# Optimization experiments

Hardware: AMD Instinct MI355X
Metric: run time of the kernel (lower is better)

## Reference

```python
import jax, jax.numpy as jnp
import numpy as np
import math

D_MODEL = 2048
B, S, PAST = 4, 2048, 2048


def setup_inputs() -> dict:
    key = jax.random.key(0)
    ks = jax.random.split(key, 8)
    scale = 0.02
    x = jax.random.normal(ks[0], (B, S, D_MODEL), dtype=jnp.float32)
    past_k = jax.random.normal(ks[1], (B, PAST, D_MODEL), dtype=jnp.float32)
    past_v = jax.random.normal(ks[2], (B, PAST, D_MODEL), dtype=jnp.float32)
    Wq = jax.random.normal(ks[3], (D_MODEL, D_MODEL), dtype=jnp.float32) * scale
    Wk = jax.random.normal(ks[4], (D_MODEL, D_MODEL), dtype=jnp.float32) * scale
    Wv = jax.random.normal(ks[5], (D_MODEL, D_MODEL), dtype=jnp.float32) * scale
    Wo = jax.random.normal(ks[6], (D_MODEL, D_MODEL), dtype=jnp.float32) * scale
    bq = jnp.zeros((D_MODEL,), jnp.float32)
    bk = jnp.zeros((D_MODEL,), jnp.float32)
    bv = jnp.zeros((D_MODEL,), jnp.float32)
    bo = jnp.zeros((D_MODEL,), jnp.float32)
    return {"x": x, "past_k": past_k, "past_v": past_v,
            "Wq": Wq, "bq": bq, "Wk": Wk, "bk": bk,
            "Wv": Wv, "bv": bv, "Wo": Wo, "bo": bo}


def reference(x, past_k, past_v, Wq, bq, Wk, bk, Wv, bv, Wo, bo):
    d_model = x.shape[-1]
    # torch Linear: y = x @ W.T + b; here W is stored [out, in] equivalently square
    q = jnp.einsum('bsd,ed->bse', x, Wq) + bq
    k = jnp.einsum('bsd,ed->bse', x, Wk) + bk
    v = jnp.einsum('bsd,ed->bse', x, Wv) + bv
    k_cache = jnp.concatenate([past_k, k], axis=1)  # [B, PAST+S, D]
    v_cache = jnp.concatenate([past_v, v], axis=1)
    scores = jnp.einsum('bqd,bkd->bqk', q, k_cache) / math.sqrt(d_model)
    weights = jax.nn.softmax(scores, axis=-1)
    attn = jnp.einsum('bqk,bkd->bqd', weights, v_cache)
    out = jnp.einsum('bqd,ed->bqe', attn, Wo) + bo
    return out, (k_cache, v_cache)
```

## Files before the change

### kernel.cpp

```cpp
#include <hip/hip_runtime.h>
#include <math.h>

typedef unsigned short u16;
typedef __bf16 bf16x8 __attribute__((ext_vector_type(8)));
typedef float f32x4 __attribute__((ext_vector_type(4)));
typedef short s16x8 __attribute__((ext_vector_type(8)));

#define DM 2048
#define NB 4
#define SEQ 2048
#define PAST_N 2048
#define CS 4096

__device__ __forceinline__ u16 f2bf(float f) {
  unsigned u = __float_as_uint(f);
  u += 0x7fff + ((u >> 16) & 1);
  return (u16)(u >> 16);
}
__device__ __forceinline__ float bf2f(u16 h) {
  return __uint_as_float(((unsigned)h) << 16);
}

__device__ __forceinline__ void gl_lds16(const u16* g, u16* l) {
  __builtin_amdgcn_global_load_lds(
      (const __attribute__((address_space(1))) unsigned*)g,
      (__attribute__((address_space(3))) unsigned*)l, 16, 0, 0);
}

__device__ __forceinline__ bf16x8 ldsfrag(const u16* s, int row, int colb) {
  const int byte_off = (row * 128 + colb) ^ ((row & 7) << 4);
  return *(const bf16x8*)((const char*)s + byte_off);
}

__device__ __forceinline__ void stage4(const u16* __restrict__ g, int ld,
                                       u16* lwb, int t) {
#pragma unroll
  for (int j = 0; j < 4; ++j) {
    const int c = j * 512 + t;
    const int row = c >> 3;
    const int slot = (c & 7) ^ (row & 7);
    gl_lds16(g + (long)row * ld + slot * 8, lwb + j * 4096);
  }
}

#define LOADA(mh)                                                       \
  _Pragma("unroll") for (int mi = 0; mi < 4; ++mi) {                    \
    const int rwa = wr * 128 + ((mh) * 4 + mi) * 16 + lr;               \
    a[mi][0] = ldsfrag(sA, rwa, kb0);                                   \
    a[mi][1] = ldsfrag(sA, rwa, 64 + kb0);                              \
  }

#define LOADB(nh)                                                       \
  _Pragma("unroll") for (int ni = 0; ni < 2; ++ni) {                    \
    const int rwb = wc * 64 + ((nh) * 2 + ni) * 16 + lr;                \
    b[ni][0] = ldsfrag(sB, rwb, kb0);                                   \
    b[ni][1] = ldsfrag(sB, rwb, 64 + kb0);                              \
  }

#define MM(mh, nh)                                                      \
  _Pragma("unroll") for (int kk = 0; kk < 2; ++kk)                      \
  _Pragma("unroll") for (int mi = 0; mi < 4; ++mi)                      \
  _Pragma("unroll") for (int ni = 0; ni < 2; ++ni)                      \
    acc[(mh) * 4 + mi][(nh) * 2 + ni] =                                 \
        __builtin_amdgcn_mfma_f32_16x16x32_bf16(                        \
            a[mi][kk], b[ni][kk], acc[(mh) * 4 + mi][(nh) * 2 + ni],    \
            0, 0, 0);

#define PHASE_SYNC                                                      \
  __builtin_amdgcn_s_barrier();                                         \
  asm volatile("s_waitcnt lgkmcnt(0)" ::: "memory");                    \
  __builtin_amdgcn_sched_barrier(0);

template <int EPI, bool REMAP>
__global__ __launch_bounds__(512, 2) void gemm256(
    const u16* __restrict__ A, const u16* __restrict__ B,
    float* __restrict__ Cf, u16* __restrict__ Cb, const float* __restrict__ bias,
    int K, int lda, int ldb, int ldc, long strA, long strB, long strC,
    float scale) {
  __shared__ __align__(16) u16 shA[2][256 * 64];
  __shared__ __align__(16) u16 shB[2][256 * 64];
  const int t = threadIdx.x;
  const int lane = t & 63;
  const int w = t >> 6;
  const int wr = w >> 2, wc = w & 3;
  const int lr = lane & 15, kb0 = (lane >> 4) * 16;

  const int gx = gridDim.x, gy = gridDim.y;
  const int nwg = gx * gy * gridDim.z;
  const int orig = blockIdx.x + gx * (blockIdx.y + gy * blockIdx.z);
  const int swz = (orig & 7) * (nwg >> 3) + (orig >> 3);
  const int bx = swz % gx;
  const int r1 = swz / gx;
  const int by = r1 % gy;
  const long bz = r1 / gy;
  const int brow = by * 256, bcol = bx * 256;

  const u16* Ab = A + bz * strA + (long)brow * lda;
  const u16* Bb = B + bz * strB + (long)bcol * ldb;

  stage4(Ab, lda, &shA[0][w * 512], t);
  stage4(Bb, ldb, &shB[0][w * 512], t);
  asm volatile("s_waitcnt vmcnt(0)" ::: "memory");
  __builtin_amdgcn_s_barrier();

  f32x4 acc[8][4] = {};
  bf16x8 a[4][2], b[2][2];
  const u16* sA;
  const u16* sB;
  const int NT = K >> 6;

  for (int tt = 0; tt < NT; ++tt) {
    const int cur = tt & 1;
    sA = shA[cur];
    sB = shB[cur];
    const bool pf = (tt + 1 < NT);
    const int ko = (tt + 1) << 6;

    LOADA(0)
    LOADB(0)
    if (pf) stage4(Ab + ko, lda, &shA[cur ^ 1][w * 512], t);
    PHASE_SYNC
    __builtin_amdgcn_s_setprio(1);
    MM(0, 0)
    __builtin_amdgcn_s_setprio(0);
    __builtin_amdgcn_s_barrier();

    LOADB(1)
    if (pf) stage4(Bb + ko, ldb, &shB[cur ^ 1][w * 512], t);
    PHASE_SYNC
    __builtin_amdgcn_s_setprio(1);
    MM(0, 1)
    __builtin_amdgcn_s_setprio(0);
    __builtin_amdgcn_s_barrier();

    LOADA(1)
    PHASE_SYNC
    __builtin_amdgcn_s_setprio(1);
    MM(1, 1)
    __builtin_amdgcn_s_setprio(0);
    __builtin_amdgcn_s_barrier();

    LOADB(0)
    PHASE_SYNC
    __builtin_amdgcn_s_setprio(1);
    MM(1, 0)
    __builtin_amdgcn_s_setprio(0);
    if (pf) asm volatile("s_waitcnt vmcnt(0)" ::: "memory");
    __builtin_amdgcn_s_barrier();
  }

  const long cb = bz * strC;
#pragma unroll
  for (int m = 0; m < 8; ++m) {
    const int r0 = wr * 128 + m * 16 + (lane >> 4) * 4;
#pragma unroll
    for (int n = 0; n < 4; ++n) {
      const int c = bcol + wc * 64 + n * 16 + lr;
      const float bv = bias ? bias[c] : 0.0f;
#pragma unroll
      for (int r = 0; r < 4; ++r) {
        const int row = brow + r0 + r;
        const long orow = REMAP ? (long)((row >> 11) * CS + PAST_N + (row & (SEQ - 1)))
                                : (long)row;
        const float val = (acc[m][n][r] + bv) * scale;
        if (EPI == 0 || EPI == 2) Cf[cb + orow * (long)ldc + c] = val;
        if (EPI == 1 || EPI == 2) Cb[cb + orow * (long)ldc + c] = f2bf(val);
      }
    }
  }
}

__global__ __launch_bounds__(256) void cast_bf16_kn(const float* __restrict__ in,
                                                    u16* __restrict__ out) {
  const int i = blockIdx.x * 256 + threadIdx.x;
  const float4 v = ((const float4*)in)[i];
  ushort4 o;
  o.x = f2bf(v.x); o.y = f2bf(v.y); o.z = f2bf(v.z); o.w = f2bf(v.w);
  ((ushort4*)out)[i] = o;
}

__global__ __launch_bounds__(256) void copy_past_kv(const float* __restrict__ pk,
                                                    const float* __restrict__ pv,
                                                    float* __restrict__ kc,
                                                    float* __restrict__ vc,
                                                    u16* __restrict__ kb) {
  const int i = blockIdx.x * 256 + threadIdx.x;
  const int d4 = DM / 4;
  const int row = i / d4;
  const int col = i - row * d4;
  const int bb = row >> 11, p = row & (PAST_N - 1);
  const long o = ((long)(bb * CS + p)) * d4 + col;
  if (blockIdx.z == 0) {
    const float4 v = ((const float4*)pk)[i];
    ((float4*)kc)[o] = v;
    ushort4 u;
    u.x = f2bf(v.x); u.y = f2bf(v.y); u.z = f2bf(v.z); u.w = f2bf(v.w);
    ((ushort4*)kb)[o] = u;
  } else {
    ((float4*)vc)[o] = ((const float4*)pv)[i];
  }
}

__global__ __launch_bounds__(256) void transpose_cast(const float* __restrict__ vcache,
                                                      u16* __restrict__ vt) {
  __shared__ float tile[32][33];
  const int bb = blockIdx.z;
  const int k0 = blockIdx.x * 32, d0 = blockIdx.y * 32;
  const int tx = threadIdx.x & 31, ty = threadIdx.x >> 5;
  const float* src = vcache + (long)bb * CS * DM;
#pragma unroll
  for (int j = 0; j < 4; ++j)
    tile[ty + 8 * j][tx] = src[(long)(k0 + ty + 8 * j) * DM + d0 + tx];
  __syncthreads();
  u16* dst = vt + (long)bb * DM * CS;
#pragma unroll
  for (int j = 0; j < 4; ++j)
    dst[(long)(d0 + ty + 8 * j) * CS + k0 + tx] = f2bf(tile[tx][ty + 8 * j]);
}

__global__ __launch_bounds__(256) void softmax_rows(u16* __restrict__ s) {
  const long row = blockIdx.x;
  u16* p = s + row * CS;
  const int t = threadIdx.x;
  const int lane = t & 63, w = t >> 6;
  float v[16];
  s16x8 c0 = ((const s16x8*)p)[t * 2];
  s16x8 c1 = ((const s16x8*)p)[t * 2 + 1];
#pragma unroll
  for (int i = 0; i < 8; ++i) {
    v[i] = bf2f((u16)c0[i]);
    v[8 + i] = bf2f((u16)c1[i]);
  }
  float m = v[0];
#pragma unroll
  for (int i = 1; i < 16; ++i) m = fmaxf(m, v[i]);
#pragma unroll
  for (int o = 32; o >= 1; o >>= 1) m = fmaxf(m, __shfl_xor(m, o, 64));
  __shared__ float red[4];
  if (lane == 0) red[w] = m;
  __syncthreads();
  m = fmaxf(fmaxf(red[0], red[1]), fmaxf(red[2], red[3]));
  float sum = 0.f;
#pragma unroll
  for (int i = 0; i < 16; ++i) {
    v[i] = __expf(v[i] - m);
    sum += v[i];
  }
#pragma unroll
  for (int o = 32; o >= 1; o >>= 1) sum += __shfl_xor(sum, o, 64);
  __syncthreads();
  if (lane == 0) red[w] = sum;
  __syncthreads();
  sum = red[0] + red[1] + red[2] + red[3];
  const float inv = 1.0f / sum;
#pragma unroll
  for (int i = 0; i < 8; ++i) {
    c0[i] = (short)f2bf(v[i] * inv);
    c1[i] = (short)f2bf(v[8 + i] * inv);
  }
  ((s16x8*)p)[t * 2] = c0;
  ((s16x8*)p)[t * 2 + 1] = c1;
}

extern "C" void kernel_launch(void* const* d_in, const int* in_sizes, int n_in,
                              void* d_out, int out_size, void* d_ws, size_t ws_size,
                              hipStream_t stream) {
  const float* x  = (const float*)d_in[0];
  const float* pk = (const float*)d_in[1];
  const float* pv = (const float*)d_in[2];
  const float* Wq = (const float*)d_in[3];
  const float* bq = (const float*)d_in[4];
  const float* Wk = (const float*)d_in[5];
  const float* bk = (const float*)d_in[6];
  const float* Wv = (const float*)d_in[7];
  const float* bv = (const float*)d_in[8];
  const float* Wo = (const float*)d_in[9];
  const float* bo = (const float*)d_in[10];

  float* out = (float*)d_out;
  float* kc = out + (long)NB * SEQ * DM;
  float* vc = kc + (long)NB * CS * DM;

  u16* ws = (u16*)d_ws;
  u16* xb  = ws;
  u16* wqb = ws + 16777216;
  u16* wkb = wqb + 4194304;
  u16* wvb = wkb + 4194304;
  u16* wob = wvb + 4194304;
  u16* qb  = ws + 33554432;
  u16* kb  = ws + 50331648;
  u16* vtb = ws + 83886080;
  u16* sc  = ws + 117440512;

  const float qscale = 0.022097086912079608f;

  cast_bf16_kn<<<16384, 256, 0, stream>>>(x, xb);
  cast_bf16_kn<<<4096, 256, 0, stream>>>(Wq, wqb);
  cast_bf16_kn<<<4096, 256, 0, stream>>>(Wk, wkb);
  cast_bf16_kn<<<4096, 256, 0, stream>>>(Wv, wvb);
  cast_bf16_kn<<<4096, 256, 0, stream>>>(Wo, wob);

  gemm256<1, false><<<dim3(8, 32, 1), 512, 0, stream>>>(
      xb, wqb, nullptr, qb, bq, 2048, 2048, 2048, 2048, 0, 0, 0, qscale);
  gemm256<2, true><<<dim3(8, 32, 1), 512, 0, stream>>>(
      xb, wkb, kc, kb, bk, 2048, 2048, 2048, 2048, 0, 0, 0, 1.0f);
  gemm256<0, true><<<dim3(8, 32, 1), 512, 0, stream>>>(
      xb, wvb, vc, nullptr, bv, 2048, 2048, 2048, 2048, 0, 0, 0, 1.0f);

  copy_past_kv<<<dim3(16384, 1, 2), 256, 0, stream>>>(pk, pv, kc, vc, kb);

  transpose_cast<<<dim3(128, 64, 4), 256, 0, stream>>>(vc, vtb);

  gemm256<1, false><<<dim3(16, 8, 4), 512, 0, stream>>>(
      qb, kb, nullptr, sc, nullptr, 2048, 2048, 2048, 4096,
      2048L * 2048, 4096L * 2048, 2048L * 4096, 1.0f);

  softmax_rows<<<8192, 256, 0, stream>>>(sc);

  gemm256<1, false><<<dim3(8, 8, 4), 512, 0, stream>>>(
      sc, vtb, nullptr, xb, nullptr, 4096, 4096, 4096, 2048,
      2048L * 4096, 2048L * 4096, 2048L * 2048, 1.0f);

  gemm256<0, false><<<dim3(8, 32, 1), 512, 0, stream>>>(
      xb, wob, out, nullptr, bo, 2048, 2048, 2048, 2048, 0, 0, 0, 1.0f);
}
```

Before: 780.1 us.

## Switch GEMM to 32x32x16 MFMA tiles and simplify the per-iteration sync

Replaces the 16x16x32 bf16 MFMA fragments with 32x32x16 MFMA, reorganising the LDS fragment loads, the accumulator layout and the epilogue row mapping to match. Each wave now reads fewer LDS fragments per unit of math. The four-phase barrier schedule with explicit waitcnts becomes a single __syncthreads per K-tile, followed by the prefetch into the other buffer. This removes barrier overhead but relies on the compiler to place the LDS and global-load waits, and it gives up the explicit overlap of loads with the MFMA phases.

```diff
diff --git a/kernel.cpp b/kernel.cpp
--- a/kernel.cpp
+++ b/kernel.cpp
@@ -4,6 +4,7 @@
 typedef unsigned short u16;
 typedef __bf16 bf16x8 __attribute__((ext_vector_type(8)));
 typedef float f32x4 __attribute__((ext_vector_type(4)));
+typedef float f32x16 __attribute__((ext_vector_type(16)));
 typedef short s16x8 __attribute__((ext_vector_type(8)));
 
 #define DM 2048
@@ -27,8 +28,8 @@
       (__attribute__((address_space(3))) unsigned*)l, 16, 0, 0);
 }
 
-__device__ __forceinline__ bf16x8 ldsfrag(const u16* s, int row, int colb) {
-  const int byte_off = (row * 128 + colb) ^ ((row & 7) << 4);
+__device__ __forceinline__ bf16x8 ldsfrag32(const u16* s, int row, int ks, int hk) {
+  const int byte_off = (row * 128 + ks * 32 + hk * 16) ^ ((row & 7) << 4);
   return *(const bf16x8*)((const char*)s + byte_off);
 }
 
@@ -43,33 +44,20 @@
   }
 }
 
-#define LOADA(mh)                                                       \
-  _Pragma("unroll") for (int mi = 0; mi < 4; ++mi) {                    \
-    const int rwa = wr * 128 + ((mh) * 4 + mi) * 16 + lr;               \
-    a[mi][0] = ldsfrag(sA, rwa, kb0);                                   \
-    a[mi][1] = ldsfrag(sA, rwa, 64 + kb0);                              \
-  }
-
-#define LOADB(nh)                                                       \
-  _Pragma("unroll") for (int ni = 0; ni < 2; ++ni) {                    \
-    const int rwb = wc * 64 + ((nh) * 2 + ni) * 16 + lr;                \
-    b[ni][0] = ldsfrag(sB, rwb, kb0);                                   \
-    b[ni][1] = ldsfrag(sB, rwb, 64 + kb0);                              \
-  }
-
-#define MM(mh, nh)                                                      \
-  _Pragma("unroll") for (int kk = 0; kk < 2; ++kk)                      \
-  _Pragma("unroll") for (int mi = 0; mi < 4; ++mi)                      \
-  _Pragma("unroll") for (int ni = 0; ni < 2; ++ni)                      \
-    acc[(mh) * 4 + mi][(nh) * 2 + ni] =                                 \
-        __builtin_amdgcn_mfma_f32_16x16x32_bf16(                        \
-            a[mi][kk], b[ni][kk], acc[(mh) * 4 + mi][(nh) * 2 + ni],    \
-            0, 0, 0);
-
-#define PHASE_SYNC                                                      \
-  __builtin_amdgcn_s_barrier();                                         \
-  asm volatile("s_waitcnt lgkmcnt(0)" ::: "memory");                    \
-  __builtin_amdgcn_sched_barrier(0);
+#define LOADA32(mh)                                                     \
+  _Pragma("unroll") for (int mi = 0; mi < 2; ++mi)                      \
+  _Pragma("unroll") for (int ks = 0; ks < 4; ++ks)                      \
+    a[mi][ks] = ldsfrag32(sA, wr * 128 + ((mh) * 2 + mi) * 32 + l31, ks, hk);
+
+#define LOADB32(nt)                                                     \
+  _Pragma("unroll") for (int ks = 0; ks < 4; ++ks)                      \
+    b[ks] = ldsfrag32(sB, wc * 64 + (nt) * 32 + l31, ks, hk);
+
+#define MM32(mh, nt)                                                    \
+  _Pragma("unroll") for (int ks = 0; ks < 4; ++ks)                      \
+  _Pragma("unroll") for (int mi = 0; mi < 2; ++mi)                      \
+    acc[(mh) * 2 + mi][nt] = __builtin_amdgcn_mfma_f32_32x32x16_bf16(   \
+        a[mi][ks], b[ks], acc[(mh) * 2 + mi][nt], 0, 0, 0);
 
 template <int EPI, bool REMAP>
 __global__ __launch_bounds__(512, 2) void gemm256(
@@ -83,7 +71,7 @@
   const int lane = t & 63;
   const int w = t >> 6;
   const int wr = w >> 2, wc = w & 3;
-  const int lr = lane & 15, kb0 = (lane >> 4) * 16;
+  const int l31 = lane & 31, hk = lane >> 5;
 
   const int gx = gridDim.x, gy = gridDim.y;
   const int nwg = gx * gy * gridDim.z;
@@ -100,69 +88,54 @@
 
   stage4(Ab, lda, &shA[0][w * 512], t);
   stage4(Bb, ldb, &shB[0][w * 512], t);
-  asm volatile("s_waitcnt vmcnt(0)" ::: "memory");
-  __builtin_amdgcn_s_barrier();
-
-  f32x4 acc[8][4] = {};
-  bf16x8 a[4][2], b[2][2];
-  const u16* sA;
-  const u16* sB;
+
+  f32x16 acc[4][2] = {};
+  bf16x8 a[2][4], b[4];
   const int NT = K >> 6;
 
   for (int tt = 0; tt < NT; ++tt) {
     const int cur = tt & 1;
-    sA = shA[cur];
-    sB = shB[cur];
-    const bool pf = (tt + 1 < NT);
-    const int ko = (tt + 1) << 6;
-
-    LOADA(0)
-    LOADB(0)
-    if (pf) stage4(Ab + ko, lda, &shA[cur ^ 1][w * 512], t);
-    PHASE_SYNC
-    __builtin_amdgcn_s_setprio(1);
-    MM(0, 0)
-    __builtin_amdgcn_s_setprio(0);
-    __builtin_amdgcn_s_barrier();
-
-    LOADB(1)
-    if (pf) stage4(Bb + ko, ldb, &shB[cur ^ 1][w * 512], t);
-    PHASE_SYNC
-    __builtin_amdgcn_s_setprio(1);
-    MM(0, 1)
-    __builtin_amdgcn_s_setprio(0);
-    __builtin_amdgcn_s_barrier();
-
-    LOADA(1)
-    PHASE_SYNC
-    __builtin_amdgcn_s_setprio(1);
-    MM(1, 1)
-    __builtin_amdgcn_s_setprio(0);
-    __builtin_amdgcn_s_barrier();
-
-    LOADB(0)
-    PHASE_SYNC
-    __builtin_amdgcn_s_setprio(1);
-    MM(1, 0)
-    __builtin_amdgcn_s_setprio(0);
-    if (pf) asm volatile("s_waitcnt vmcnt(0)" ::: "memory");
-    __builtin_amdgcn_s_barrier();
+    __syncthreads();
+    if (tt + 1 < NT) {
+      const int ko = (tt + 1) << 6;
+      stage4(Bb + ko, ldb, &shB[cur ^ 1][w * 512], t);
+      stage4(Ab + ko, lda, &shA[cur ^ 1][w * 512], t);
+    }
+    const u16* sA = shA[cur];
+    const u16* sB = shB[cur];
+
+    LOADA32(0)
+    LOADB32(0)
+    __builtin_amdgcn_s_setprio(1);
+    MM32(0, 0)
+    __builtin_amdgcn_s_setprio(0);
+    LOADB32(1)
+    __builtin_amdgcn_s_setprio(1);
+    MM32(0, 1)
+    __builtin_amdgcn_s_setprio(0);
+    LOADA32(1)
+    __builtin_amdgcn_s_setprio(1);
+    MM32(1, 1)
+    __builtin_amdgcn_s_setprio(0);
+    LOADB32(0)
+    __builtin_amdgcn_s_setprio(1);
+    MM32(1, 0)
+    __builtin_amdgcn_s_setprio(0);
   }
 
   const long cb = bz * strC;
 #pragma unroll
-  for (int m = 0; m < 8; ++m) {
-    const int r0 = wr * 128 + m * 16 + (lane >> 4) * 4;
-#pragma unroll
-    for (int n = 0; n < 4; ++n) {
-      const int c = bcol + wc * 64 + n * 16 + lr;
+  for (int mi = 0; mi < 4; ++mi) {
+#pragma unroll
+    for (int nt = 0; nt < 2; ++nt) {
+      const int c = bcol + wc * 64 + nt * 32 + l31;
       const float bv = bias ? bias[c] : 0.0f;
 #pragma unroll
-      for (int r = 0; r < 4; ++r) {
-        const int row = brow + r0 + r;
+      for (int r = 0; r < 16; ++r) {
+        const int row = brow + wr * 128 + mi * 32 + 8 * (r >> 2) + 4 * hk + (r & 3);
         const long orow = REMAP ? (long)((row >> 11) * CS + PAST_N + (row & (SEQ - 1)))
                                 : (long)row;
-        const float val = (acc[m][n][r] + bv) * scale;
+        const float val = (acc[mi][nt][r] + bv) * scale;
         if (EPI == 0 || EPI == 2) Cf[cb + orow * (long)ldc + c] = val;
         if (EPI == 1 || EPI == 2) Cb[cb + orow * (long)ldc + c] = f2bf(val);
       }
```

New measurement: 806.8 us. +3.4%, slower.

## Fuse QKV projections into one launch and write transposed V directly

Applied to the files above, without the earlier changes.

Merges the three Q/K/V projection GEMMs into one kernel with a z-dimension selecting the weight, bias and epilogue. The V branch writes the transposed bf16 V straight into the V^T buffer, and only the past V is transposed from the input. This removes the full transpose pass over the whole V cache and two kernel launches, and gives one larger grid. The cost is a strided ushort4 store pattern for V^T in the GEMM epilogue and a branchy epilogue.

```diff
diff --git a/kernel.cpp b/kernel.cpp
--- a/kernel.cpp
+++ b/kernel.cpp
@@ -71,7 +71,48 @@
   asm volatile("s_waitcnt lgkmcnt(0)" ::: "memory");                    \
   __builtin_amdgcn_sched_barrier(0);
 
-template <int EPI, bool REMAP>
+#define GEMM_MAIN_LOOP(Abp, Bbp, ldav, ldbv)                            \
+  stage4(Abp, ldav, &shA[0][w * 512], t);                               \
+  stage4(Bbp, ldbv, &shB[0][w * 512], t);                               \
+  asm volatile("s_waitcnt vmcnt(0)" ::: "memory");                      \
+  __builtin_amdgcn_s_barrier();                                         \
+  for (int tt = 0; tt < NT; ++tt) {                                     \
+    const int cur = tt & 1;                                             \
+    const u16* sA = shA[cur];                                           \
+    const u16* sB = shB[cur];                                           \
+    const bool pf = (tt + 1 < NT);                                      \
+    const int ko = (tt + 1) << 6;                                       \
+    LOADA(0)                                                            \
+    LOADB(0)                                                            \
+    if (pf) stage4(Abp + ko, ldav, &shA[cur ^ 1][w * 512], t);          \
+    PHASE_SYNC                                                          \
+    __builtin_amdgcn_s_setprio(1);                                      \
+    MM(0, 0)                                                            \
+    __builtin_amdgcn_s_setprio(0);                                      \
+    __builtin_amdgcn_s_barrier();                                       \
+    LOADB(1)                                                            \
+    if (pf) stage4(Bbp + ko, ldbv, &shB[cur ^ 1][w * 512], t);          \
+    PHASE_SYNC                                                          \
+    __builtin_amdgcn_s_setprio(1);                                      \
+    MM(0, 1)                                                            \
+    __builtin_amdgcn_s_setprio(0);                                      \
+    __builtin_amdgcn_s_barrier();                                       \
+    LOADA(1)                                                            \
+    PHASE_SYNC                                                          \
+    __builtin_amdgcn_s_setprio(1);                                      \
+    MM(1, 1)                                                            \
+    __builtin_amdgcn_s_setprio(0);                                      \
+    __builtin_amdgcn_s_barrier();                                       \
+    LOADB(0)                                                            \
+    PHASE_SYNC                                                          \
+    __builtin_amdgcn_s_setprio(1);                                      \
+    MM(1, 0)                                                            \
+    __builtin_amdgcn_s_setprio(0);                                      \
+    if (pf) asm volatile("s_waitcnt vmcnt(0)" ::: "memory");            \
+    __builtin_amdgcn_s_barrier();                                       \
+  }
+
+template <int EPI>
 __global__ __launch_bounds__(512, 2) void gemm256(
     const u16* __restrict__ A, const u16* __restrict__ B,
     float* __restrict__ Cf, u16* __restrict__ Cb, const float* __restrict__ bias,
@@ -97,57 +138,12 @@
 
   const u16* Ab = A + bz * strA + (long)brow * lda;
   const u16* Bb = B + bz * strB + (long)bcol * ldb;
-
-  stage4(Ab, lda, &shA[0][w * 512], t);
-  stage4(Bb, ldb, &shB[0][w * 512], t);
-  asm volatile("s_waitcnt vmcnt(0)" ::: "memory");
-  __builtin_amdgcn_s_barrier();
+  const int NT = K >> 6;
 
   f32x4 acc[8][4] = {};
   bf16x8 a[4][2], b[2][2];
-  const u16* sA;
-  const u16* sB;
-  const int NT = K >> 6;
-
-  for (int tt = 0; tt < NT; ++tt) {
-    const int cur = tt & 1;
-    sA = shA[cur];
-    sB = shB[cur];
-    const bool pf = (tt + 1 < NT);
-    const int ko = (tt + 1) << 6;
-
-    LOADA(0)
-    LOADB(0)
-    if (pf) stage4(Ab + ko, lda, &shA[cur ^ 1][w * 512], t);
-    PHASE_SYNC
-    __builtin_amdgcn_s_setprio(1);
-    MM(0, 0)
-    __builtin_amdgcn_s_setprio(0);
-    __builtin_amdgcn_s_barrier();
-
-    LOADB(1)
-    if (pf) stage4(Bb + ko, ldb, &shB[cur ^ 1][w * 512], t);
-    PHASE_SYNC
-    __builtin_amdgcn_s_setprio(1);
-    MM(0, 1)
-    __builtin_amdgcn_s_setprio(0);
-    __builtin_amdgcn_s_barrier();
-
-    LOADA(1)
-    PHASE_SYNC
-    __builtin_amdgcn_s_setprio(1);
-    MM(1, 1)
-    __builtin_amdgcn_s_setprio(0);
-    __builtin_amdgcn_s_barrier();
-
-    LOADB(0)
-    PHASE_SYNC
-    __builtin_amdgcn_s_setprio(1);
-    MM(1, 0)
-    __builtin_amdgcn_s_setprio(0);
-    if (pf) asm volatile("s_waitcnt vmcnt(0)" ::: "memory");
-    __builtin_amdgcn_s_barrier();
-  }
+
+  GEMM_MAIN_LOOP(Ab, Bb, lda, ldb)
 
   const long cb = bz * strC;
 #pragma unroll
@@ -160,11 +156,103 @@
 #pragma unroll
       for (int r = 0; r < 4; ++r) {
         const int row = brow + r0 + r;
-        const long orow = REMAP ? (long)((row >> 11) * CS + PAST_N + (row & (SEQ - 1)))
-                                : (long)row;
         const float val = (acc[m][n][r] + bv) * scale;
-        if (EPI == 0 || EPI == 2) Cf[cb + orow * (long)ldc + c] = val;
-        if (EPI == 1 || EPI == 2) Cb[cb + orow * (long)ldc + c] = f2bf(val);
+        if (EPI == 0) Cf[cb + (long)row * ldc + c] = val;
+        else          Cb[cb + (long)row * ldc + c] = f2bf(val);
+      }
+    }
+  }
+}
+
+__global__ __launch_bounds__(512, 2) void gemm_qkv(
+    const u16* __restrict__ A, const u16* __restrict__ wq,
+    const u16* __restrict__ wk, const u16* __restrict__ wv,
+    const float* __restrict__ bq, const float* __restrict__ bk,
+    const float* __restrict__ bv_, u16* __restrict__ qb,
+    float* __restrict__ kc, u16* __restrict__ kbm,
+    float* __restrict__ vc, u16* __restrict__ vtb, float qscale) {
+  __shared__ __align__(16) u16 shA[2][256 * 64];
+  __shared__ __align__(16) u16 shB[2][256 * 64];
+  const int t = threadIdx.x;
+  const int lane = t & 63;
+  const int w = t >> 6;
+  const int wr = w >> 2, wc = w & 3;
+  const int lr = lane & 15, kb0 = (lane >> 4) * 16;
+
+  const int gx = gridDim.x, gy = gridDim.y;
+  const int nwg = gx * gy * gridDim.z;
+  const int orig = blockIdx.x + gx * (blockIdx.y + gy * blockIdx.z);
+  const int swz = (orig & 7) * (nwg >> 3) + (orig >> 3);
+  const int bx = swz % gx;
+  const int r1 = swz / gx;
+  const int by = r1 % gy;
+  const int bz = r1 / gy;
+  const int brow = by * 256, bcol = bx * 256;
+
+  const u16* Bw = (bz == 0) ? wq : (bz == 1) ? wk : wv;
+  const float* bias = (bz == 0) ? bq : (bz == 1) ? bk : bv_;
+  const u16* Ab = A + (long)brow * 2048;
+  const u16* Bb = Bw + (long)bcol * 2048;
+  const int NT = 2048 >> 6;
+
+  f32x4 acc[8][4] = {};
+  bf16x8 a[4][2], b[2][2];
+
+  GEMM_MAIN_LOOP(Ab, Bb, 2048, 2048)
+
+  if (bz == 0) {
+#pragma unroll
+    for (int m = 0; m < 8; ++m) {
+      const int r0 = wr * 128 + m * 16 + (lane >> 4) * 4;
+#pragma unroll
+      for (int n = 0; n < 4; ++n) {
+        const int c = bcol + wc * 64 + n * 16 + lr;
+        const float bvv = bias[c];
+#pragma unroll
+        for (int r = 0; r < 4; ++r) {
+          const int row = brow + r0 + r;
+          qb[(long)row * 2048 + c] = f2bf((acc[m][n][r] + bvv) * qscale);
+        }
+      }
+    }
+  } else if (bz == 1) {
+#pragma unroll
+    for (int m = 0; m < 8; ++m) {
+      const int r0 = wr * 128 + m * 16 + (lane >> 4) * 4;
+#pragma unroll
+      for (int n = 0; n < 4; ++n) {
+        const int c = bcol + wc * 64 + n * 16 + lr;
+        const float bvv = bias[c];
+#pragma unroll
+        for (int r = 0; r < 4; ++r) {
+          const int row = brow + r0 + r;
+          const long orow = (long)((row >> 11) * CS + PAST_N + (row & (SEQ - 1)));
+          const float val = acc[m][n][r] + bvv;
+          kc[orow * 2048 + c] = val;
+          kbm[orow * 2048 + c] = f2bf(val);
+        }
+      }
+    }
+  } else {
+#pragma unroll
+    for (int m = 0; m < 8; ++m) {
+      const int r0 = wr * 128 + m * 16 + (lane >> 4) * 4;
+#pragma unroll
+      for (int n = 0; n < 4; ++n) {
+        const int c = bcol + wc * 64 + n * 16 + lr;
+        const float bvv = bias[c];
+        ushort4 pk4;
+        const int row0 = brow + r0;
+        const int bat = row0 >> 11;
+        const long orow0 = (long)(bat * CS + PAST_N + (row0 & (SEQ - 1)));
+#pragma unroll
+        for (int r = 0; r < 4; ++r) {
+          const float val = acc[m][n][r] + bvv;
+          vc[(orow0 + r) * 2048 + c] = val;
+          ((u16*)&pk4)[r] = f2bf(val);
+        }
+        *(ushort4*)(vtb + (long)bat * DM * CS + (long)c * CS + PAST_N +
+                    (row0 & (SEQ - 1))) = pk4;
       }
     }
   }
@@ -201,13 +289,13 @@
   }
 }
 
-__global__ __launch_bounds__(256) void transpose_cast(const float* __restrict__ vcache,
+__global__ __launch_bounds__(256) void transpose_past(const float* __restrict__ pv,
                                                       u16* __restrict__ vt) {
   __shared__ float tile[32][33];
   const int bb = blockIdx.z;
   const int k0 = blockIdx.x * 32, d0 = blockIdx.y * 32;
   const int tx = threadIdx.x & 31, ty = threadIdx.x >> 5;
-  const float* src = vcache + (long)bb * CS * DM;
+  const float* src = pv + (long)bb * PAST_N * DM;
 #pragma unroll
   for (int j = 0; j < 4; ++j)
     tile[ty + 8 * j][tx] = src[(long)(k0 + ty + 8 * j) * DM + d0 + tx];
@@ -300,27 +388,23 @@
   cast_bf16_kn<<<4096, 256, 0, stream>>>(Wv, wvb);
   cast_bf16_kn<<<4096, 256, 0, stream>>>(Wo, wob);
 
-  gemm256<1, false><<<dim3(8, 32, 1), 512, 0, stream>>>(
-      xb, wqb, nullptr, qb, bq, 2048, 2048, 2048, 2048, 0, 0, 0, qscale);
-  gemm256<2, true><<<dim3(8, 32, 1), 512, 0, stream>>>(
-      xb, wkb, kc, kb, bk, 2048, 2048, 2048, 2048, 0, 0, 0, 1.0f);
-  gemm256<0, true><<<dim3(8, 32, 1), 512, 0, stream>>>(
-      xb, wvb, vc, nullptr, bv, 2048, 2048, 2048, 2048, 0, 0, 0, 1.0f);
+  transpose_past<<<dim3(64, 64, 4), 256, 0, stream>>>(pv, vtb);
+
+  gemm_qkv<<<dim3(8, 32, 3), 512, 0, stream>>>(
+      xb, wqb, wkb, wvb, bq, bk, bv, qb, kc, kb, vc, vtb, qscale);
 
   copy_past_kv<<<dim3(16384, 1, 2), 256, 0, stream>>>(pk, pv, kc, vc, kb);
 
-  transpose_cast<<<dim3(128, 64, 4), 256, 0, stream>>>(vc, vtb);
-
-  gemm256<1, false><<<dim3(16, 8, 4), 512, 0, stream>>>(
+  gemm256<1><<<dim3(16, 8, 4), 512, 0, stream>>>(
       qb, kb, nullptr, sc, nullptr, 2048, 2048, 2048, 4096,
       2048L * 2048, 4096L * 2048, 2048L * 4096, 1.0f);
 
   softmax_rows<<<8192, 256, 0, stream>>>(sc);
 
-  gemm256<1, false><<<dim3(8, 8, 4), 512, 0, stream>>>(
+  gemm256<1><<<dim3(8, 8, 4), 512, 0, stream>>>(
       sc, vtb, nullptr, xb, nullptr, 4096, 4096, 4096, 2048,
       2048L * 4096, 2048L * 4096, 2048L * 2048, 1.0f);
 
-  gemm256<0, false><<<dim3(8, 32, 1), 512, 0, stream>>>(
+  gemm256<0><<<dim3(8, 32, 1), 512, 0, stream>>>(
       xb, wob, out, nullptr, bo, 2048, 2048, 2048, 2048, 0, 0, 0, 1.0f);
 }
```

Result: faster. 756.9 us (-3.0%).
